# Performance work log

Hardware: AMD Instinct MI355X
Metric: run time of the kernel (lower is better)

## Reference

```python
import jax, jax.numpy as jnp
import numpy as np

N_NODES = 50000
N_EDGES = 800000
N_GRAPHS = 256
D = 256
L = 3
BN_EPS = 1e-5


def setup_inputs() -> dict:
    key = jax.random.key(0)
    ks = jax.random.split(key, 8)
    x = jax.random.normal(ks[0], (N_NODES, D), dtype=jnp.float32)
    edge_index = jax.random.randint(ks[1], (2, N_EDGES), 0, N_NODES, dtype=jnp.int64)
    batch = jnp.sort(jax.random.randint(ks[2], (N_NODES,), 0, N_GRAPHS, dtype=jnp.int64))
    # small init scale keeps ReLU/BN chain numerically tame
    w1 = jax.random.normal(ks[3], (L, D, D), dtype=jnp.float32) * 0.05
    b1 = jnp.zeros((L, D), dtype=jnp.float32)
    w2 = jax.random.normal(ks[4], (L, D, D), dtype=jnp.float32) * 0.05
    b2 = jnp.zeros((L, D), dtype=jnp.float32)
    gamma = jnp.ones((L, D), dtype=jnp.float32)
    beta = jnp.zeros((L, D), dtype=jnp.float32)
    return {"x": x, "edge_index": edge_index, "batch": batch,
            "w1": w1, "b1": b1, "w2": w2, "b2": b2,
            "gamma": gamma, "beta": beta}


def reference(x, edge_index, batch, w1, b1, w2, b2, gamma, beta):
    src = edge_index[0]  # message senders (x_j)
    dst = edge_index[1]  # aggregation targets (x_i)
    h = x
    xs = []
    for i in range(L):
        # GINConv (eps=0): MLP(x_i + sum_{j in N(i)} x_j)
        agg = jax.ops.segment_sum(h[src], dst, num_segments=N_NODES)  # [N, D]
        z = h + agg
        z = jnp.maximum(z @ w1[i] + b1[i], 0.0) @ w2[i] + b2[i]  # Linear-ReLU-Linear
        z = jnp.maximum(z, 0.0)  # F.relu after conv
        # BatchNorm1d (training mode: biased batch stats over nodes)
        mean = jnp.mean(z, axis=0)
        var = jnp.var(z, axis=0)
        z = (z - mean) * jax.lax.rsqrt(var + BN_EPS) * gamma[i] + beta[i]
        xs.append(z)
        h = z
    # global_add_pool per layer, then concat along features -> [G, L*D]
    pooled = [jax.ops.segment_sum(xi, batch, num_segments=N_GRAPHS) for xi in xs]
    return jnp.concatenate(pooled, axis=1)
```

## Files before the change

### kernel.cpp

```cpp
#include <hip/hip_runtime.h>

#define NN 50000
#define NE 800000
#define NG 256
#define DD 256
#define NL 3
#define BN_EPS 1e-5f
#define MPAD 50048
#define CAP 96
#define NMB 391

typedef short bf16x8 __attribute__((ext_vector_type(8)));
typedef float f32x4 __attribute__((ext_vector_type(4)));
typedef unsigned short ushort8 __attribute__((ext_vector_type(8)));

__device__ __forceinline__ unsigned short f2bf(float f) {
    unsigned int u = __float_as_uint(f);
    u += 0x7FFFu + ((u >> 16) & 1u);
    return (unsigned short)(u >> 16);
}
__device__ __forceinline__ float bf2f(unsigned short s) {
    return __uint_as_float(((unsigned int)s) << 16);
}

__global__ void k_init(int* __restrict__ deg) {
    int i = blockIdx.x * blockDim.x + threadIdx.x;
    if (i < NN) deg[i] = 0;
}

__global__ void k_scatter(const int* __restrict__ ei, int* __restrict__ deg,
                          unsigned short* __restrict__ elist) {
    int e = blockIdx.x * blockDim.x + threadIdx.x;
    if (e >= NE) return;
    int s = ei[e];
    int d = ei[NE + e];
    int pos = atomicAdd(&deg[d], 1);
    elist[(size_t)d * CAP + pos] = (unsigned short)s;
}

__global__ void k_gbounds(const int* __restrict__ batch, int* __restrict__ gstart) {
    int g = threadIdx.x;
    int lo = 0, hi = NN;
    while (lo < hi) {
        int mid = (lo + hi) >> 1;
        if (batch[mid] < g) lo = mid + 1; else hi = mid;
    }
    gstart[g] = lo;
    if (g == 0) gstart[NG] = NN;
}

__global__ void k_f2bf(const float* __restrict__ in, unsigned short* __restrict__ out, int n4) {
    int i = blockIdx.x * blockDim.x + threadIdx.x;
    if (i >= n4) return;
    float4 v = ((const float4*)in)[i];
    ushort4 o;
    o.x = f2bf(v.x); o.y = f2bf(v.y); o.z = f2bf(v.z); o.w = f2bf(v.w);
    ((ushort4*)out)[i] = o;
}

__global__ void k_zrow(unsigned short* __restrict__ hbf) {
    hbf[(size_t)NN * DD + threadIdx.x] = 0;
}

__global__ void k_zpad(unsigned short* p) {
    int i = blockIdx.x * blockDim.x + threadIdx.x;
    const int total = (MPAD - NN) * DD;
    if (i < total) p[NN * DD + i] = 0;
}

__global__ void k_wconv(const float* __restrict__ w1, const float* __restrict__ w2,
                        unsigned short* __restrict__ wt) {
    int flat = blockIdx.x * blockDim.x + threadIdx.x;
    if (flat >= 6 * 65536) return;
    int mat = flat >> 16;
    int n = (flat >> 8) & 255;
    int k = flat & 255;
    const float* src = (mat < 3) ? (w1 + ((size_t)mat << 16)) : (w2 + ((size_t)(mat - 3) << 16));
    wt[flat] = f2bf(src[k * 256 + n]);
}

__global__ __launch_bounds__(256) void k_agg_bf(const unsigned short* __restrict__ h,
                                                const int* __restrict__ deg,
                                                const unsigned short* __restrict__ elist,
                                                unsigned short* __restrict__ z0) {
    int wave = threadIdx.x >> 6;
    int lane = threadIdx.x & 63;
    int node = blockIdx.x * 4 + wave;
    int chunk = lane & 31;
    int half = lane >> 5;
    const ushort8* h8 = (const ushort8*)h;

    float acc[8];
    if (half == 0) {
        ushort8 own = h8[(size_t)node * 32 + chunk];
        #pragma unroll
        for (int j = 0; j < 8; ++j) acc[j] = bf2f(own[j]);
    } else {
        #pragma unroll
        for (int j = 0; j < 8; ++j) acc[j] = 0.f;
    }

    int n = deg[node];
    const unsigned short* el = elist + (size_t)node * CAP;
    int i = 0;
    for (; i + 8 <= n; i += 8) {
        ushort8 sv = *(const ushort8*)(el + i);
        int i0 = half ? sv[1] : sv[0];
        int i1 = half ? sv[3] : sv[2];
        int i2 = half ? sv[5] : sv[4];
        int i3 = half ? sv[7] : sv[6];
        ushort8 r0 = h8[(size_t)i0 * 32 + chunk];
        ushort8 r1 = h8[(size_t)i1 * 32 + chunk];
        ushort8 r2 = h8[(size_t)i2 * 32 + chunk];
        ushort8 r3 = h8[(size_t)i3 * 32 + chunk];
        #pragma unroll
        for (int j = 0; j < 8; ++j) acc[j] += bf2f(r0[j]);
        #pragma unroll
        for (int j = 0; j < 8; ++j) acc[j] += bf2f(r1[j]);
        #pragma unroll
        for (int j = 0; j < 8; ++j) acc[j] += bf2f(r2[j]);
        #pragma unroll
        for (int j = 0; j < 8; ++j) acc[j] += bf2f(r3[j]);
    }
    for (; i < n; i += 2) {
        int s0 = el[i];
        int s1 = (i + 1 < n) ? (int)el[i + 1] : NN;
        int idx = half ? s1 : s0;
        ushort8 r = h8[(size_t)idx * 32 + chunk];
        #pragma unroll
        for (int j = 0; j < 8; ++j) acc[j] += bf2f(r[j]);
    }

    ushort8 o;
    #pragma unroll
    for (int j = 0; j < 8; ++j) {
        float other = __shfl_xor(acc[j], 32);
        o[j] = f2bf(acc[j] + other);
    }
    if (half == 0) ((ushort8*)z0)[(size_t)node * 32 + chunk] = o;
}

#define GBM 128
#define GBK 64
template<int OUT_BF16, int STATS>
__global__ __launch_bounds__(256) void k_mfma_gemm(const unsigned short* __restrict__ A,
                                                   const unsigned short* __restrict__ BT,
                                                   const float* __restrict__ bias,
                                                   void* __restrict__ Cout,
                                                   float* __restrict__ pstat) {
    __shared__ short As[GBM * GBK];
    __shared__ short Bs[GBM * GBK];
    __shared__ float spart[2][128][2];
    int tid = threadIdx.x;
    int lane = tid & 63;
    int wave = tid >> 6;
    int wr = wave >> 1, wc = wave & 1;
    long m0 = (long)blockIdx.x * GBM;
    int n0 = blockIdx.y * GBM;
    const int r = lane & 15, hi = lane >> 4;

    f32x4 acc[4][4];
    #pragma unroll
    for (int m = 0; m < 4; ++m)
        #pragma unroll
        for (int n = 0; n < 4; ++n)
            acc[m][n] = (f32x4){0.f, 0.f, 0.f, 0.f};

    for (int k0 = 0; k0 < DD; k0 += GBK) {
        #pragma unroll
        for (int p = 0; p < 4; ++p) {
            int flat = p * 256 + tid;
            int row = flat >> 3;
            int c8 = flat & 7;
            int slot = c8 ^ (row & 7);
            bf16x8 va = *(const bf16x8*)(A + (m0 + row) * DD + k0 + c8 * 8);
            *(bf16x8*)(As + row * GBK + slot * 8) = va;
            bf16x8 vb = *(const bf16x8*)(BT + (long)(n0 + row) * DD + k0 + c8 * 8);
            *(bf16x8*)(Bs + row * GBK + slot * 8) = vb;
        }
        __syncthreads();

        bf16x8 af[4][2], bfr[4][2];
        #pragma unroll
        for (int m = 0; m < 4; ++m) {
            int row = wr * 64 + m * 16 + r;
            #pragma unroll
            for (int kk = 0; kk < 2; ++kk) {
                int slot = (kk * 4 + hi) ^ (row & 7);
                af[m][kk] = *(const bf16x8*)(As + row * GBK + slot * 8);
            }
        }
        #pragma unroll
        for (int n = 0; n < 4; ++n) {
            int col = wc * 64 + n * 16 + r;
            #pragma unroll
            for (int kk = 0; kk < 2; ++kk) {
                int slot = (kk * 4 + hi) ^ (col & 7);
                bfr[n][kk] = *(const bf16x8*)(Bs + col * GBK + slot * 8);
            }
        }
        #pragma unroll
        for (int kk = 0; kk < 2; ++kk)
            #pragma unroll
            for (int m = 0; m < 4; ++m)
                #pragma unroll
                for (int n = 0; n < 4; ++n)
                    acc[m][n] = __builtin_amdgcn_mfma_f32_16x16x32_bf16(af[m][kk], bfr[n][kk], acc[m][n], 0, 0, 0);
        __syncthreads();
    }

    #pragma unroll
    for (int n = 0; n < 4; ++n) {
        int col = n0 + wc * 64 + n * 16 + r;
        float bv = bias[col];
        float cs = 0.f, cs2 = 0.f;
        #pragma unroll
        for (int m = 0; m < 4; ++m) {
            #pragma unroll
            for (int j = 0; j < 4; ++j) {
                long grow = m0 + wr * 64 + m * 16 + hi * 4 + j;
                float v = acc[m][n][j] + bv;
                v = v > 0.f ? v : 0.f;
                if (OUT_BF16) ((unsigned short*)Cout)[grow * DD + col] = f2bf(v);
                else          ((float*)Cout)[grow * DD + col] = v;
                if (STATS) {
                    float vm = (grow < NN) ? v : 0.f;
                    cs += vm; cs2 += vm * vm;
                }
            }
        }
        if (STATS) {
            cs  += __shfl_xor(cs, 16);  cs  += __shfl_xor(cs, 32);
            cs2 += __shfl_xor(cs2, 16); cs2 += __shfl_xor(cs2, 32);
            if (hi == 0) {
                spart[wr][wc * 64 + n * 16 + r][0] = cs;
                spart[wr][wc * 64 + n * 16 + r][1] = cs2;
            }
        }
    }
    if (STATS) {
        __syncthreads();
        if (tid < 128) {
            float s  = spart[0][tid][0] + spart[1][tid][0];
            float s2 = spart[0][tid][1] + spart[1][tid][1];
            pstat[(size_t)blockIdx.x * 512 + n0 + tid] = s;
            pstat[(size_t)blockIdx.x * 512 + 256 + n0 + tid] = s2;
        }
    }
}

__global__ __launch_bounds__(256) void k_bnscale2(const float* __restrict__ pstat,
                                                  const float* __restrict__ gamma,
                                                  const float* __restrict__ beta,
                                                  float* __restrict__ ss) {
    int c = blockIdx.x;
    int t = threadIdx.x;
    float s = 0.f, s2 = 0.f;
    for (int mb = t; mb < NMB; mb += 256) {
        s  += pstat[(size_t)mb * 512 + c];
        s2 += pstat[(size_t)mb * 512 + 256 + c];
    }
    __shared__ float rs[256], rs2[256];
    rs[t] = s; rs2[t] = s2;
    __syncthreads();
    #pragma unroll
    for (int d = 128; d > 0; d >>= 1) {
        if (t < d) { rs[t] += rs[t + d]; rs2[t] += rs2[t + d]; }
        __syncthreads();
    }
    if (t == 0) {
        float mean = rs[0] * (1.0f / NN);
        float var = rs2[0] * (1.0f / NN) - mean * mean;
        float sc = gamma[c] * rsqrtf(var + BN_EPS);
        ss[c] = sc;
        ss[DD + c] = beta[c] - mean * sc;
    }
}

__global__ __launch_bounds__(512) void k_bnpool(const float* __restrict__ z,
                                                const float* __restrict__ ss,
                                                const int* __restrict__ gstart,
                                                unsigned short* __restrict__ hbf,
                                                float* __restrict__ out, int layer) {
    __shared__ float4 red[8][64];
    int g = blockIdx.x;
    int t = threadIdx.x;
    int q = t & 63, rg = t >> 6;
    float4 sc = ((const float4*)ss)[q];
    float4 sh = ((const float4*)(ss + DD))[q];
    int lo = gstart[g], hi = gstart[g + 1];
    float4 s = {0.f, 0.f, 0.f, 0.f};
    const float4* z4 = (const float4*)z;
    ushort4* h4 = (ushort4*)hbf;
    for (int r = lo + rg; r < hi; r += 8) {
        float4 v = z4[r * 64 + q];
        v.x = v.x * sc.x + sh.x;
        v.y = v.y * sc.y + sh.y;
        v.z = v.z * sc.z + sh.z;
        v.w = v.w * sc.w + sh.w;
        s.x += v.x; s.y += v.y; s.z += v.z; s.w += v.w;
        ushort4 o;
        o.x = f2bf(v.x); o.y = f2bf(v.y); o.z = f2bf(v.z); o.w = f2bf(v.w);
        h4[r * 64 + q] = o;
    }
    red[rg][q] = s;
    __syncthreads();
    if (rg < 4) {
        float4 a = red[rg][q], b = red[rg + 4][q];
        a.x += b.x; a.y += b.y; a.z += b.z; a.w += b.w;
        red[rg][q] = a;
    }
    __syncthreads();
    if (rg < 2) {
        float4 a = red[rg][q], b = red[rg + 2][q];
        a.x += b.x; a.y += b.y; a.z += b.z; a.w += b.w;
        red[rg][q] = a;
    }
    __syncthreads();
    if (rg == 0) {
        float4 a = red[0][q], b = red[1][q];
        a.x += b.x; a.y += b.y; a.z += b.z; a.w += b.w;
        ((float4*)(out + (size_t)g * (NL * DD) + layer * DD))[q] = a;
    }
}

extern "C" void kernel_launch(void* const* d_in, const int* in_sizes, int n_in,
                              void* d_out, int out_size, void* d_ws, size_t ws_size,
                              hipStream_t stream) {
    const float* x     = (const float*)d_in[0];
    const int*   ei    = (const int*)d_in[1];
    const int*   batch = (const int*)d_in[2];
    const float* w1    = (const float*)d_in[3];
    const float* b1    = (const float*)d_in[4];
    const float* w2    = (const float*)d_in[5];
    const float* b2    = (const float*)d_in[6];
    const float* gamma = (const float*)d_in[7];
    const float* beta  = (const float*)d_in[8];
    float* out = (float*)d_out;

    char* ws = (char*)d_ws;
    size_t off = 0;
    auto alloc = [&](size_t bytes) -> void* {
        void* p = ws + off;
        off += (bytes + 255) & ~size_t(255);
        return p;
    };
    float*          buf0 = (float*)alloc((size_t)MPAD * DD * 4);
    unsigned short* zbf  = (unsigned short*)alloc((size_t)MPAD * DD * 2);
    unsigned short* h1bf = (unsigned short*)alloc((size_t)MPAD * DD * 2);
    unsigned short* hbf  = (unsigned short*)alloc((size_t)(NN + 64) * DD * 2);
    unsigned short* wt   = (unsigned short*)alloc((size_t)6 * DD * DD * 2);
    int* deg    = (int*)alloc((size_t)NN * 4);
    unsigned short* elist = (unsigned short*)alloc((size_t)NN * CAP * 2);
    int* gstart = (int*)alloc((size_t)(NG + 1) * 4);
    float* pstat = (float*)alloc((size_t)NMB * 512 * 4);
    float* ss   = (float*)alloc(2 * DD * 4);

    k_init<<<(NN + 255) / 256, 256, 0, stream>>>(deg);
    k_scatter<<<(NE + 255) / 256, 256, 0, stream>>>(ei, deg, elist);
    k_gbounds<<<1, 256, 0, stream>>>(batch, gstart);

    k_wconv<<<(6 * 65536 + 255) / 256, 256, 0, stream>>>(w1, w2, wt);
    k_f2bf<<<(NN * DD / 4 + 255) / 256, 256, 0, stream>>>(x, hbf, NN * DD / 4);
    k_zrow<<<1, 256, 0, stream>>>(hbf);
    k_zpad<<<((MPAD - NN) * DD + 255) / 256, 256, 0, stream>>>(zbf);

    dim3 ggrid(MPAD / GBM, DD / GBM);
    for (int l = 0; l < NL; ++l) {
        k_agg_bf<<<NN / 4, 256, 0, stream>>>(hbf, deg, elist, zbf);
        k_mfma_gemm<1, 0><<<ggrid, 256, 0, stream>>>(zbf, wt + (size_t)l * DD * DD, b1 + l * DD, h1bf, nullptr);
        k_mfma_gemm<0, 1><<<ggrid, 256, 0, stream>>>(h1bf, wt + (size_t)(3 + l) * DD * DD, b2 + l * DD, buf0, pstat);
        k_bnscale2<<<DD, 256, 0, stream>>>(pstat, gamma + l * DD, beta + l * DD, ss);
        k_bnpool<<<NG, 512, 0, stream>>>(buf0, ss, gstart, hbf, out, l);
    }
}
```

Baseline: 450.2 us.

## Fuse the two MLP GEMMs into one kernel keeping the hidden tile in LDS

The Linear-ReLU-Linear pair is merged into a single kernel. Each block of 512 threads computes a 128-row strip across all 256 columns, stores the bf16 ReLU hidden activations in a swizzled 64KB LDS buffer, and runs the second GEMM straight from LDS. This removes the h1 global write and read round trip and one launch per layer. In exchange LDS use per block rises to about 120KB, which limits occupancy, and the grid drops to 391 blocks.

After: 419.9 us. -6.7%, faster.

```diff
diff --git a/kernel.cpp b/kernel.cpp
--- a/kernel.cpp
+++ b/kernel.cpp
@@ -140,23 +140,22 @@
     if (half == 0) ((ushort8*)z0)[(size_t)node * 32 + chunk] = o;
 }
 
-#define GBM 128
-#define GBK 64
-template<int OUT_BF16, int STATS>
-__global__ __launch_bounds__(256) void k_mfma_gemm(const unsigned short* __restrict__ A,
-                                                   const unsigned short* __restrict__ BT,
-                                                   const float* __restrict__ bias,
-                                                   void* __restrict__ Cout,
-                                                   float* __restrict__ pstat) {
-    __shared__ short As[GBM * GBK];
-    __shared__ short Bs[GBM * GBK];
-    __shared__ float spart[2][128][2];
+__global__ __launch_bounds__(512, 2) void k_mlp(const unsigned short* __restrict__ A,
+                                                const unsigned short* __restrict__ BT1,
+                                                const unsigned short* __restrict__ BT2,
+                                                const float* __restrict__ b1,
+                                                const float* __restrict__ b2,
+                                                float* __restrict__ Cout,
+                                                float* __restrict__ pstat) {
+    __shared__ short As[128 * 64];
+    __shared__ short Bs[256 * 64];
+    __shared__ short H1[128 * 256];
+    __shared__ float spart[2][256][2];
     int tid = threadIdx.x;
     int lane = tid & 63;
     int wave = tid >> 6;
-    int wr = wave >> 1, wc = wave & 1;
-    long m0 = (long)blockIdx.x * GBM;
-    int n0 = blockIdx.y * GBM;
+    int wr = wave >> 2, wc = wave & 3;
+    long m0 = (long)blockIdx.x * 128;
     const int r = lane & 15, hi = lane >> 4;
 
     f32x4 acc[4][4];
@@ -166,20 +165,24 @@
         for (int n = 0; n < 4; ++n)
             acc[m][n] = (f32x4){0.f, 0.f, 0.f, 0.f};
 
-    for (int k0 = 0; k0 < DD; k0 += GBK) {
+    for (int k0 = 0; k0 < DD; k0 += 64) {
+        #pragma unroll
+        for (int p = 0; p < 2; ++p) {
+            int flat = p * 512 + tid;
+            int row = flat >> 3, c8 = flat & 7;
+            int slot = c8 ^ (row & 7);
+            *(bf16x8*)(As + row * 64 + slot * 8) =
+                *(const bf16x8*)(A + (m0 + row) * DD + k0 + c8 * 8);
+        }
         #pragma unroll
         for (int p = 0; p < 4; ++p) {
-            int flat = p * 256 + tid;
-            int row = flat >> 3;
-            int c8 = flat & 7;
+            int flat = p * 512 + tid;
+            int row = flat >> 3, c8 = flat & 7;
             int slot = c8 ^ (row & 7);
-            bf16x8 va = *(const bf16x8*)(A + (m0 + row) * DD + k0 + c8 * 8);
-            *(bf16x8*)(As + row * GBK + slot * 8) = va;
-            bf16x8 vb = *(const bf16x8*)(BT + (long)(n0 + row) * DD + k0 + c8 * 8);
-            *(bf16x8*)(Bs + row * GBK + slot * 8) = vb;
+            *(bf16x8*)(Bs + row * 64 + slot * 8) =
+                *(const bf16x8*)(BT1 + (long)row * DD + k0 + c8 * 8);
         }
         __syncthreads();
-
         bf16x8 af[4][2], bfr[4][2];
         #pragma unroll
         for (int m = 0; m < 4; ++m) {
@@ -187,7 +190,7 @@
             #pragma unroll
             for (int kk = 0; kk < 2; ++kk) {
                 int slot = (kk * 4 + hi) ^ (row & 7);
-                af[m][kk] = *(const bf16x8*)(As + row * GBK + slot * 8);
+                af[m][kk] = *(const bf16x8*)(As + row * 64 + slot * 8);
             }
         }
         #pragma unroll
@@ -196,7 +199,7 @@
             #pragma unroll
             for (int kk = 0; kk < 2; ++kk) {
                 int slot = (kk * 4 + hi) ^ (col & 7);
-                bfr[n][kk] = *(const bf16x8*)(Bs + col * GBK + slot * 8);
+                bfr[n][kk] = *(const bf16x8*)(Bs + col * 64 + slot * 8);
             }
         }
         #pragma unroll
@@ -211,8 +214,70 @@
 
     #pragma unroll
     for (int n = 0; n < 4; ++n) {
-        int col = n0 + wc * 64 + n * 16 + r;
-        float bv = bias[col];
+        int col = wc * 64 + n * 16 + r;
+        float bv = b1[col];
+        int g = col >> 3, j8 = col & 7;
+        #pragma unroll
+        for (int m = 0; m < 4; ++m) {
+            #pragma unroll
+            for (int j = 0; j < 4; ++j) {
+                int row = wr * 64 + m * 16 + hi * 4 + j;
+                float v = acc[m][n][j] + bv;
+                v = v > 0.f ? v : 0.f;
+                H1[row * 256 + (g ^ (row & 7)) * 8 + j8] = (short)f2bf(v);
+            }
+        }
+    }
+    #pragma unroll
+    for (int m = 0; m < 4; ++m)
+        #pragma unroll
+        for (int n = 0; n < 4; ++n)
+            acc[m][n] = (f32x4){0.f, 0.f, 0.f, 0.f};
+    __syncthreads();
+
+    for (int k0 = 0; k0 < DD; k0 += 64) {
+        #pragma unroll
+        for (int p = 0; p < 4; ++p) {
+            int flat = p * 512 + tid;
+            int row = flat >> 3, c8 = flat & 7;
+            int slot = c8 ^ (row & 7);
+            *(bf16x8*)(Bs + row * 64 + slot * 8) =
+                *(const bf16x8*)(BT2 + (long)row * DD + k0 + c8 * 8);
+        }
+        __syncthreads();
+        bf16x8 af[4][2], bfr[4][2];
+        #pragma unroll
+        for (int m = 0; m < 4; ++m) {
+            int row = wr * 64 + m * 16 + r;
+            #pragma unroll
+            for (int kk = 0; kk < 2; ++kk) {
+                int g = (k0 >> 3) + kk * 4 + hi;
+                af[m][kk] = *(const bf16x8*)(H1 + row * 256 + (g ^ (row & 7)) * 8);
+            }
+        }
+        #pragma unroll
+        for (int n = 0; n < 4; ++n) {
+            int col = wc * 64 + n * 16 + r;
+            #pragma unroll
+            for (int kk = 0; kk < 2; ++kk) {
+                int slot = (kk * 4 + hi) ^ (col & 7);
+                bfr[n][kk] = *(const bf16x8*)(Bs + col * 64 + slot * 8);
+            }
+        }
+        #pragma unroll
+        for (int kk = 0; kk < 2; ++kk)
+            #pragma unroll
+            for (int m = 0; m < 4; ++m)
+                #pragma unroll
+                for (int n = 0; n < 4; ++n)
+                    acc[m][n] = __builtin_amdgcn_mfma_f32_16x16x32_bf16(af[m][kk], bfr[n][kk], acc[m][n], 0, 0, 0);
+        __syncthreads();
+    }
+
+    #pragma unroll
+    for (int n = 0; n < 4; ++n) {
+        int col = wc * 64 + n * 16 + r;
+        float bv = b2[col];
         float cs = 0.f, cs2 = 0.f;
         #pragma unroll
         for (int m = 0; m < 4; ++m) {
@@ -221,31 +286,24 @@
                 long grow = m0 + wr * 64 + m * 16 + hi * 4 + j;
                 float v = acc[m][n][j] + bv;
                 v = v > 0.f ? v : 0.f;
-                if (OUT_BF16) ((unsigned short*)Cout)[grow * DD + col] = f2bf(v);
-                else          ((float*)Cout)[grow * DD + col] = v;
-                if (STATS) {
-                    float vm = (grow < NN) ? v : 0.f;
-                    cs += vm; cs2 += vm * vm;
-                }
-            }
-        }
-        if (STATS) {
-            cs  += __shfl_xor(cs, 16);  cs  += __shfl_xor(cs, 32);
-            cs2 += __shfl_xor(cs2, 16); cs2 += __shfl_xor(cs2, 32);
-            if (hi == 0) {
-                spart[wr][wc * 64 + n * 16 + r][0] = cs;
-                spart[wr][wc * 64 + n * 16 + r][1] = cs2;
-            }
-        }
-    }
-    if (STATS) {
-        __syncthreads();
-        if (tid < 128) {
-            float s  = spart[0][tid][0] + spart[1][tid][0];
-            float s2 = spart[0][tid][1] + spart[1][tid][1];
-            pstat[(size_t)blockIdx.x * 512 + n0 + tid] = s;
-            pstat[(size_t)blockIdx.x * 512 + 256 + n0 + tid] = s2;
-        }
+                Cout[grow * DD + col] = v;
+                float vm = (grow < NN) ? v : 0.f;
+                cs += vm; cs2 += vm * vm;
+            }
+        }
+        cs  += __shfl_xor(cs, 16);  cs  += __shfl_xor(cs, 32);
+        cs2 += __shfl_xor(cs2, 16); cs2 += __shfl_xor(cs2, 32);
+        if (hi == 0) {
+            spart[wr][col][0] = cs;
+            spart[wr][col][1] = cs2;
+        }
+    }
+    __syncthreads();
+    if (tid < 256) {
+        float s  = spart[0][tid][0] + spart[1][tid][0];
+        float s2 = spart[0][tid][1] + spart[1][tid][1];
+        pstat[(size_t)blockIdx.x * 512 + tid] = s;
+        pstat[(size_t)blockIdx.x * 512 + 256 + tid] = s2;
     }
 }
 
@@ -347,7 +405,6 @@
     };
     float*          buf0 = (float*)alloc((size_t)MPAD * DD * 4);
     unsigned short* zbf  = (unsigned short*)alloc((size_t)MPAD * DD * 2);
-    unsigned short* h1bf = (unsigned short*)alloc((size_t)MPAD * DD * 2);
     unsigned short* hbf  = (unsigned short*)alloc((size_t)(NN + 64) * DD * 2);
     unsigned short* wt   = (unsigned short*)alloc((size_t)6 * DD * DD * 2);
     int* deg    = (int*)alloc((size_t)NN * 4);
@@ -365,11 +422,11 @@
     k_zrow<<<1, 256, 0, stream>>>(hbf);
     k_zpad<<<((MPAD - NN) * DD + 255) / 256, 256, 0, stream>>>(zbf);
 
-    dim3 ggrid(MPAD / GBM, DD / GBM);
     for (int l = 0; l < NL; ++l) {
         k_agg_bf<<<NN / 4, 256, 0, stream>>>(hbf, deg, elist, zbf);
-        k_mfma_gemm<1, 0><<<ggrid, 256, 0, stream>>>(zbf, wt + (size_t)l * DD * DD, b1 + l * DD, h1bf, nullptr);
-        k_mfma_gemm<0, 1><<<ggrid, 256, 0, stream>>>(h1bf, wt + (size_t)(3 + l) * DD * DD, b2 + l * DD, buf0, pstat);
+        k_mlp<<<NMB, 512, 0, stream>>>(zbf, wt + (size_t)l * DD * DD,
+                                       wt + (size_t)(3 + l) * DD * DD,
+                                       b1 + l * DD, b2 + l * DD, buf0, pstat);
         k_bnscale2<<<DD, 256, 0, stream>>>(pstat, gamma + l * DD, beta + l * DD, ss);
         k_bnpool<<<NG, 512, 0, stream>>>(buf0, ss, gstart, hbf, out, l);
     }
```
